# Kernel optimization log

Measured on AMD Instinct MI355X. Metric: run time of the kernel, lower is better.

The kernel has to match this reference:

```python
import jax, jax.numpy as jnp
import numpy as np

N = 100000        # vertices
E = 20000         # hyperedges
NNZ = 1000000     # incidence pairs
IN_CH = 128
HEADS = 8
OUT_CH = 16
D = HEADS * OUT_CH  # 128
NUM_TYPES = 16
K_CURV = 1.0      # Lorentz k = 1/c with c = 1


def lorentz_linear(x, W, b, scale_log):
    # HyboNet LorentzLinear: linear map, then project onto hyperboloid.
    y = x @ W.T + b                                   # [N, D]
    time = jax.nn.sigmoid(y[..., :1]) * jnp.exp(scale_log) + 1.1  # [N, 1]
    x_narrow = y[..., 1:]                             # [N, D-1]
    sq = jnp.sum(x_narrow * x_narrow, axis=-1, keepdims=True)
    scale = (time * time - K_CURV) / (sq + 1e-8)
    return jnp.concatenate([time, x_narrow * jnp.sqrt(scale)], axis=-1)


def setup_inputs() -> dict:
    key = jax.random.key(0)
    ks = jax.random.split(key, 8)
    X = jax.random.normal(ks[0], (N, IN_CH), dtype=jnp.float32)
    emb_ty = jax.random.normal(ks[1], (NUM_TYPES, D), dtype=jnp.float32)
    vertex = jax.random.randint(ks[2], (NNZ,), 0, N, dtype=jnp.int32)
    edges = jax.random.randint(ks[3], (NNZ,), 0, E, dtype=jnp.int32)
    type_ids = jax.random.randint(ks[4], (NNZ,), 0, NUM_TYPES, dtype=jnp.int32)
    # LorentzLinear params (nn.Linear with bias, scale init log(10))
    W = jax.random.normal(ks[5], (D, IN_CH), dtype=jnp.float32) / np.sqrt(IN_CH)
    b = jnp.zeros((D,), dtype=jnp.float32)
    scale_log = jnp.asarray(np.log(10.0), dtype=jnp.float32)
    eps = jnp.asarray([0.5], dtype=jnp.float32)
    return {"X": X, "emb_ty": emb_ty, "W": W, "b": b, "scale_log": scale_log,
            "eps": eps, "vertex": vertex, "edges": edges, "type_ids": type_ids,
            "num_edges": E}


def reference(X, emb_ty, W, b, scale_log, eps, vertex, edges, type_ids, num_edges):
    n = X.shape[0]
    Xh = lorentz_linear(X, W, b, scale_log)           # [N, D]
    Xve = Xh[vertex] - emb_ty[type_ids]               # [NNZ, D] gather + subtract
    Xe = jax.ops.segment_sum(Xve, edges, num_segments=num_edges)  # [E, D]
    Xev = Xe[edges]                                   # [NNZ, D]
    Xv = jax.ops.segment_sum(Xev, vertex, num_segments=n)         # [N, D]
    return eps * Xv + Xh
```

## Files before the change

### kernel.cpp

```cpp
#include <hip/hip_runtime.h>
#include <hip/hip_bf16.h>


#define E_SEGS 20000

__global__ __launch_bounds__(256) void lorentz_gemm_kernel(
    const float* __restrict__ X, const float* __restrict__ W,
    const float* __restrict__ bias, const float* __restrict__ scale_log,
    float* __restrict__ Xh, int N)
{
    __shared__ float Wt[128][132];
    __shared__ float Xs[128][64];
    const int t = threadIdx.x;

    #pragma unroll
    for (int i = 0; i < 16; ++i) {
        int f4 = t + i * 256;
        int d  = f4 >> 5;
        int k0 = (f4 & 31) << 2;
        float4 w = ((const float4*)W)[f4];
        Wt[k0+0][d] = w.x; Wt[k0+1][d] = w.y;
        Wt[k0+2][d] = w.z; Wt[k0+3][d] = w.w;
    }
    const int row0 = blockIdx.x * 64;
    #pragma unroll
    for (int i = 0; i < 8; ++i) {
        int f4 = t + i * 256;
        int r  = f4 >> 5;
        int k0 = (f4 & 31) << 2;
        int gr = row0 + r;
        float4 x = make_float4(0.f, 0.f, 0.f, 0.f);
        if (gr < N) x = ((const float4*)X)[(size_t)gr * 32 + (f4 & 31)];
        Xs[k0+0][r] = x.x; Xs[k0+1][r] = x.y;
        Xs[k0+2][r] = x.z; Xs[k0+3][r] = x.w;
    }
    __syncthreads();

    const int rg = t >> 4;
    const int cg = t & 15;
    const int cb = cg << 3;

    float acc[4][8];
    #pragma unroll
    for (int r = 0; r < 4; ++r)
        #pragma unroll
        for (int j = 0; j < 8; ++j) acc[r][j] = 0.f;

    #pragma unroll 4
    for (int k = 0; k < 128; ++k) {
        float4 xr = *(const float4*)&Xs[k][rg << 2];
        float4 w0 = *(const float4*)&Wt[k][cb];
        float4 w1 = *(const float4*)&Wt[k][cb + 4];
        #pragma unroll
        for (int r = 0; r < 4; ++r) {
            float xv = (&xr.x)[r];
            acc[r][0] += xv * w0.x; acc[r][1] += xv * w0.y;
            acc[r][2] += xv * w0.z; acc[r][3] += xv * w0.w;
            acc[r][4] += xv * w1.x; acc[r][5] += xv * w1.y;
            acc[r][6] += xv * w1.z; acc[r][7] += xv * w1.w;
        }
    }

    float4 b0 = ((const float4*)bias)[cg * 2];
    float4 b1 = ((const float4*)bias)[cg * 2 + 1];
    #pragma unroll
    for (int r = 0; r < 4; ++r) {
        acc[r][0] += b0.x; acc[r][1] += b0.y; acc[r][2] += b0.z; acc[r][3] += b0.w;
        acc[r][4] += b1.x; acc[r][5] += b1.y; acc[r][6] += b1.z; acc[r][7] += b1.w;
    }

    const float es = expf(scale_log[0]);

    #pragma unroll
    for (int r = 0; r < 4; ++r) {
        float sq = 0.f;
        #pragma unroll
        for (int j = 0; j < 8; ++j) sq += acc[r][j] * acc[r][j];
        if (cg == 0) sq -= acc[r][0] * acc[r][0];
        #pragma unroll
        for (int m = 1; m < 16; m <<= 1) sq += __shfl_xor(sq, m, 16);
        float y0   = __shfl(acc[r][0], 0, 16);
        float time = es / (1.f + expf(-y0)) + 1.1f;
        float ss   = sqrtf((time * time - 1.f) / (sq + 1e-8f));
        float4 o0, o1;
        o0.x = (cg == 0) ? time : acc[r][0] * ss;
        o0.y = acc[r][1] * ss; o0.z = acc[r][2] * ss; o0.w = acc[r][3] * ss;
        o1.x = acc[r][4] * ss; o1.y = acc[r][5] * ss;
        o1.z = acc[r][6] * ss; o1.w = acc[r][7] * ss;
        int grow = row0 + (rg << 2) + r;
        if (grow < N) {
            float4* ph = (float4*)(Xh + (size_t)grow * 128 + cb);
            ph[0] = o0; ph[1] = o1;
        }
    }
}

__global__ __launch_bounds__(256) void count_both_kernel(
    const int* __restrict__ edges, const int* __restrict__ vertex,
    int* __restrict__ hist_e, int* __restrict__ hist_v, int n)
{
    int i = blockIdx.x * 256 + threadIdx.x;
    if (i < n) {
        atomicAdd(&hist_e[edges[i]], 1);
        atomicAdd(&hist_v[vertex[i]], 1);
    }
}

__global__ __launch_bounds__(1024) void scan_kernel(
    const int* __restrict__ counts, int* __restrict__ offs, int n)
{
    __shared__ int buf[1024];
    __shared__ int s_carry;
    const int tid = threadIdx.x;
    if (tid == 0) s_carry = 0;
    __syncthreads();
    for (int base = 0; base < n; base += 4096) {
        int i0 = base + tid * 4;
        int c0 = (i0 + 0 < n) ? counts[i0 + 0] : 0;
        int c1 = (i0 + 1 < n) ? counts[i0 + 1] : 0;
        int c2 = (i0 + 2 < n) ? counts[i0 + 2] : 0;
        int c3 = (i0 + 3 < n) ? counts[i0 + 3] : 0;
        int s = c0 + c1 + c2 + c3;
        buf[tid] = s;
        __syncthreads();
        for (int off = 1; off < 1024; off <<= 1) {
            int t = (tid >= off) ? buf[tid - off] : 0;
            __syncthreads();
            buf[tid] += t;
            __syncthreads();
        }
        int incl  = buf[tid];
        int total = buf[1023];
        int carry = s_carry;
        int ex = carry + incl - s;
        if (i0 + 0 < n) offs[i0 + 0] = ex;
        if (i0 + 1 < n) offs[i0 + 1] = ex + c0;
        if (i0 + 2 < n) offs[i0 + 2] = ex + c0 + c1;
        if (i0 + 3 < n) offs[i0 + 3] = ex + c0 + c1 + c2;
        __syncthreads();
        if (tid == 0) s_carry = carry + total;
        __syncthreads();
    }
    if (tid == 0) offs[n] = s_carry;
}

__global__ __launch_bounds__(256) void fill_both_kernel(
    const int* __restrict__ edges, const int* __restrict__ vertex,
    const int* __restrict__ types,
    const int* __restrict__ offs_e, int* __restrict__ cur_e,
    int* __restrict__ vals_e,
    const int* __restrict__ offs_v, int* __restrict__ cur_v,
    int* __restrict__ segs_v, int n)
{
    int i = blockIdx.x * 256 + threadIdx.x;
    if (i < n) {
        int s = edges[i];
        int v = vertex[i];
        int pe = atomicAdd(&cur_e[s], 1);
        vals_e[offs_e[s] + pe] = v | (types[i] << 17);
        int pv = atomicAdd(&cur_v[v], 1);
        segs_v[offs_v[v] + pv] = s;
    }
}

__global__ __launch_bounds__(256) void edge_gather_kernel(
    const float* __restrict__ Xh, const float* __restrict__ emb,
    const int* __restrict__ offs, const int* __restrict__ vals,
    float* __restrict__ Xe, int nsegs)
{
    int seg = blockIdx.x * 4 + (threadIdx.x >> 6);
    if (seg >= nsegs) return;
    int lane = threadIdx.x & 63;
    int beg = offs[seg], end = offs[seg + 1];
    float2 acc = make_float2(0.f, 0.f);
    int e = beg;
    for (; e + 1 < end; e += 2) {
        int p0 = vals[e], p1 = vals[e + 1];
        int v0 = p0 & 0x1FFFF, t0 = p0 >> 17;
        int v1 = p1 & 0x1FFFF, t1 = p1 >> 17;
        float2 a  = ((const float2*)Xh)[(size_t)v0 * 64 + lane];
        float2 b  = ((const float2*)Xh)[(size_t)v1 * 64 + lane];
        float2 m0 = ((const float2*)emb)[t0 * 64 + lane];
        float2 m1 = ((const float2*)emb)[t1 * 64 + lane];
        acc.x += (a.x - m0.x) + (b.x - m1.x);
        acc.y += (a.y - m0.y) + (b.y - m1.y);
    }
    if (e < end) {
        int p0 = vals[e];
        int v0 = p0 & 0x1FFFF, t0 = p0 >> 17;
        float2 a  = ((const float2*)Xh)[(size_t)v0 * 64 + lane];
        float2 m0 = ((const float2*)emb)[t0 * 64 + lane];
        acc.x += a.x - m0.x;
        acc.y += a.y - m0.y;
    }
    ((float2*)Xe)[(size_t)seg * 64 + lane] = acc;
}

__global__ __launch_bounds__(256) void vertex_gather_kernel(
    const float* __restrict__ Xh, const float* __restrict__ Xe,
    const int* __restrict__ offs, const int* __restrict__ segs,
    const float* __restrict__ eps, float* __restrict__ out, int N)
{
    int v = blockIdx.x * 4 + (threadIdx.x >> 6);
    if (v >= N) return;
    int lane = threadIdx.x & 63;
    int beg = offs[v], end = offs[v + 1];
    float2 acc = make_float2(0.f, 0.f);
    int e = beg;
    for (; e + 1 < end; e += 2) {
        int s0 = segs[e], s1 = segs[e + 1];
        float2 a = ((const float2*)Xe)[(size_t)s0 * 64 + lane];
        float2 b = ((const float2*)Xe)[(size_t)s1 * 64 + lane];
        acc.x += a.x + b.x;
        acc.y += a.y + b.y;
    }
    if (e < end) {
        int s0 = segs[e];
        float2 a = ((const float2*)Xe)[(size_t)s0 * 64 + lane];
        acc.x += a.x;
        acc.y += a.y;
    }
    float ep = eps[0];
    float2 xh = ((const float2*)Xh)[(size_t)v * 64 + lane];
    float2 o;
    o.x = xh.x + ep * acc.x;
    o.y = xh.y + ep * acc.y;
    ((float2*)out)[(size_t)v * 64 + lane] = o;
}

extern "C" void kernel_launch(void* const* d_in, const int* in_sizes, int n_in,
                              void* d_out, int out_size, void* d_ws, size_t ws_size,
                              hipStream_t stream) {
    const float* X         = (const float*)d_in[0];
    const float* emb_ty    = (const float*)d_in[1];
    const float* W         = (const float*)d_in[2];
    const float* bias      = (const float*)d_in[3];
    const float* scale_log = (const float*)d_in[4];
    const float* eps       = (const float*)d_in[5];
    const int*   vertex    = (const int*)d_in[6];
    const int*   edges     = (const int*)d_in[7];
    const int*   type_ids  = (const int*)d_in[8];

    const int N   = in_sizes[0] / 128;
    const int nnz = in_sizes[6];
    const int E   = E_SEGS;

    float* Xh = (float*)d_ws;
    float* Xe = Xh + (size_t)N * 128;
    int* ip      = (int*)(Xe + (size_t)E * 128);
    int* offs_e  = ip;              ip += E + 1;
    int* offs_v  = ip;              ip += N + 1;
    int* hist_e  = ip;              ip += E;
    int* hist_v  = ip;              ip += N;
    int* cur_e   = ip;              ip += E;
    int* cur_v   = ip;              ip += N;
    int* vals_e  = ip;              ip += nnz;
    int* segs_v  = ip;              ip += nnz;

    hipMemsetAsync(hist_e, 0, (size_t)(2 * E + 2 * N) * sizeof(int), stream);

    float* out = (float*)d_out;
    int blocks_nnz = (nnz + 255) / 256;

    count_both_kernel<<<blocks_nnz, 256, 0, stream>>>(
        edges, vertex, hist_e, hist_v, nnz);
    scan_kernel<<<1, 1024, 0, stream>>>(hist_e, offs_e, E);
    scan_kernel<<<1, 1024, 0, stream>>>(hist_v, offs_v, N);
    fill_both_kernel<<<blocks_nnz, 256, 0, stream>>>(
        edges, vertex, type_ids, offs_e, cur_e, vals_e, offs_v, cur_v,
        segs_v, nnz);

    lorentz_gemm_kernel<<<(N + 63) / 64, 256, 0, stream>>>(
        X, W, bias, scale_log, Xh, N);

    edge_gather_kernel<<<(E + 3) / 4, 256, 0, stream>>>(
        Xh, emb_ty, offs_e, vals_e, Xe, E);

    vertex_gather_kernel<<<(N + 3) / 4, 256, 0, stream>>>(
        Xh, Xe, offs_v, segs_v, eps, out, N);
}
```

Baseline: 717.5 us.

## Parallelize prefix scans, swizzle GEMM smem, and widen gather loads to float4

The single-block scans over the edge and vertex histograms are replaced by a three-phase multi-block scan: partial scans, a scan of block sums, then an add pass. The GEMM now stores W and X row-major in shared memory as float4, with an XOR swizzle on W and padding on X, and computes dot products over k in groups of four. The edge and vertex gather kernels switch from float2 to float4 loads, with each half-wave taking alternate incidences and a shuffle combining the two halves. The scan change removes a serialized one-block bottleneck at the cost of extra launches, and the gather change halves the number of load instructions per row.

```diff
diff --git a/kernel.cpp b/kernel.cpp
--- a/kernel.cpp
+++ b/kernel.cpp
@@ -9,58 +9,59 @@
     const float* __restrict__ bias, const float* __restrict__ scale_log,
     float* __restrict__ Xh, int N)
 {
-    __shared__ float Wt[128][132];
-    __shared__ float Xs[128][64];
+    __shared__ float4 Ws[128 * 32];
+    __shared__ float4 Xs[64 * 33];
     const int t = threadIdx.x;
 
     #pragma unroll
     for (int i = 0; i < 16; ++i) {
         int f4 = t + i * 256;
         int d  = f4 >> 5;
-        int k0 = (f4 & 31) << 2;
-        float4 w = ((const float4*)W)[f4];
-        Wt[k0+0][d] = w.x; Wt[k0+1][d] = w.y;
-        Wt[k0+2][d] = w.z; Wt[k0+3][d] = w.w;
+        int c  = f4 & 31;
+        Ws[d * 32 + (c ^ ((d >> 3) & 7))] = ((const float4*)W)[f4];
     }
     const int row0 = blockIdx.x * 64;
     #pragma unroll
     for (int i = 0; i < 8; ++i) {
         int f4 = t + i * 256;
         int r  = f4 >> 5;
-        int k0 = (f4 & 31) << 2;
+        int c  = f4 & 31;
         int gr = row0 + r;
         float4 x = make_float4(0.f, 0.f, 0.f, 0.f);
-        if (gr < N) x = ((const float4*)X)[(size_t)gr * 32 + (f4 & 31)];
-        Xs[k0+0][r] = x.x; Xs[k0+1][r] = x.y;
-        Xs[k0+2][r] = x.z; Xs[k0+3][r] = x.w;
+        if (gr < N) x = ((const float4*)X)[(size_t)gr * 32 + c];
+        Xs[r * 33 + c] = x;
     }
     __syncthreads();
 
-    const int rg = t >> 4;
-    const int cg = t & 15;
+    const int rg  = t >> 4;
+    const int cg  = t & 15;
+    const int r0  = rg << 2;
+    const int swz = cg & 7;
+
+    float acc[4][8];
+    #pragma unroll
+    for (int r = 0; r < 4; ++r)
+        #pragma unroll
+        for (int j = 0; j < 8; ++j) acc[r][j] = 0.f;
+
+    #pragma unroll 2
+    for (int k4 = 0; k4 < 32; ++k4) {
+        float4 xq[4];
+        #pragma unroll
+        for (int rr = 0; rr < 4; ++rr) xq[rr] = Xs[(r0 + rr) * 33 + k4];
+        float4 wq[8];
+        const int kk = k4 ^ swz;
+        #pragma unroll
+        for (int j = 0; j < 8; ++j) wq[j] = Ws[(cg * 8 + j) * 32 + kk];
+        #pragma unroll
+        for (int rr = 0; rr < 4; ++rr)
+            #pragma unroll
+            for (int j = 0; j < 8; ++j)
+                acc[rr][j] += xq[rr].x * wq[j].x + xq[rr].y * wq[j].y
+                            + xq[rr].z * wq[j].z + xq[rr].w * wq[j].w;
+    }
+
     const int cb = cg << 3;
-
-    float acc[4][8];
-    #pragma unroll
-    for (int r = 0; r < 4; ++r)
-        #pragma unroll
-        for (int j = 0; j < 8; ++j) acc[r][j] = 0.f;
-
-    #pragma unroll 4
-    for (int k = 0; k < 128; ++k) {
-        float4 xr = *(const float4*)&Xs[k][rg << 2];
-        float4 w0 = *(const float4*)&Wt[k][cb];
-        float4 w1 = *(const float4*)&Wt[k][cb + 4];
-        #pragma unroll
-        for (int r = 0; r < 4; ++r) {
-            float xv = (&xr.x)[r];
-            acc[r][0] += xv * w0.x; acc[r][1] += xv * w0.y;
-            acc[r][2] += xv * w0.z; acc[r][3] += xv * w0.w;
-            acc[r][4] += xv * w1.x; acc[r][5] += xv * w1.y;
-            acc[r][6] += xv * w1.z; acc[r][7] += xv * w1.w;
-        }
-    }
-
     float4 b0 = ((const float4*)bias)[cg * 2];
     float4 b1 = ((const float4*)bias)[cg * 2 + 1];
     #pragma unroll
@@ -87,7 +88,7 @@
         o0.y = acc[r][1] * ss; o0.z = acc[r][2] * ss; o0.w = acc[r][3] * ss;
         o1.x = acc[r][4] * ss; o1.y = acc[r][5] * ss;
         o1.z = acc[r][6] * ss; o1.w = acc[r][7] * ss;
-        int grow = row0 + (rg << 2) + r;
+        int grow = row0 + r0 + r;
         if (grow < N) {
             float4* ph = (float4*)(Xh + (size_t)grow * 128 + cb);
             ph[0] = o0; ph[1] = o1;
@@ -106,42 +107,66 @@
     }
 }
 
-__global__ __launch_bounds__(1024) void scan_kernel(
-    const int* __restrict__ counts, int* __restrict__ offs, int n)
-{
-    __shared__ int buf[1024];
-    __shared__ int s_carry;
+__global__ __launch_bounds__(256) void scan_partial_kernel(
+    const int* __restrict__ counts, int* __restrict__ offs,
+    int* __restrict__ bsums, int n)
+{
+    __shared__ int buf[256];
+    const int b = blockIdx.x, tid = threadIdx.x;
+    const int i0 = b * 1024 + tid * 4;
+    int c0 = (i0 + 0 < n) ? counts[i0 + 0] : 0;
+    int c1 = (i0 + 1 < n) ? counts[i0 + 1] : 0;
+    int c2 = (i0 + 2 < n) ? counts[i0 + 2] : 0;
+    int c3 = (i0 + 3 < n) ? counts[i0 + 3] : 0;
+    int s = c0 + c1 + c2 + c3;
+    buf[tid] = s;
+    __syncthreads();
+    #pragma unroll
+    for (int off = 1; off < 256; off <<= 1) {
+        int v = (tid >= off) ? buf[tid - off] : 0;
+        __syncthreads();
+        buf[tid] += v;
+        __syncthreads();
+    }
+    int ex = buf[tid] - s;
+    if (i0 + 0 < n) offs[i0 + 0] = ex;
+    if (i0 + 1 < n) offs[i0 + 1] = ex + c0;
+    if (i0 + 2 < n) offs[i0 + 2] = ex + c0 + c1;
+    if (i0 + 3 < n) offs[i0 + 3] = ex + c0 + c1 + c2;
+    if (tid == 255) bsums[b] = buf[255];
+}
+
+__global__ __launch_bounds__(256) void scan_bsums_kernel(
+    int* __restrict__ bsums, int nb)
+{
+    __shared__ int buf[256];
     const int tid = threadIdx.x;
-    if (tid == 0) s_carry = 0;
+    int v = (tid < nb) ? bsums[tid] : 0;
+    buf[tid] = v;
     __syncthreads();
-    for (int base = 0; base < n; base += 4096) {
-        int i0 = base + tid * 4;
-        int c0 = (i0 + 0 < n) ? counts[i0 + 0] : 0;
-        int c1 = (i0 + 1 < n) ? counts[i0 + 1] : 0;
-        int c2 = (i0 + 2 < n) ? counts[i0 + 2] : 0;
-        int c3 = (i0 + 3 < n) ? counts[i0 + 3] : 0;
-        int s = c0 + c1 + c2 + c3;
-        buf[tid] = s;
+    #pragma unroll
+    for (int off = 1; off < 256; off <<= 1) {
+        int u = (tid >= off) ? buf[tid - off] : 0;
         __syncthreads();
-        for (int off = 1; off < 1024; off <<= 1) {
-            int t = (tid >= off) ? buf[tid - off] : 0;
-            __syncthreads();
-            buf[tid] += t;
-            __syncthreads();
-        }
-        int incl  = buf[tid];
-        int total = buf[1023];
-        int carry = s_carry;
-        int ex = carry + incl - s;
-        if (i0 + 0 < n) offs[i0 + 0] = ex;
-        if (i0 + 1 < n) offs[i0 + 1] = ex + c0;
-        if (i0 + 2 < n) offs[i0 + 2] = ex + c0 + c1;
-        if (i0 + 3 < n) offs[i0 + 3] = ex + c0 + c1 + c2;
+        buf[tid] += u;
         __syncthreads();
-        if (tid == 0) s_carry = carry + total;
-        __syncthreads();
-    }
-    if (tid == 0) offs[n] = s_carry;
+    }
+    if (tid < nb) bsums[tid] = buf[tid] - v;
+}
+
+__global__ __launch_bounds__(256) void scan_add_kernel(
+    int* __restrict__ offs, const int* __restrict__ bsums, int n, int total)
+{
+    const int b = blockIdx.x, tid = threadIdx.x;
+    const int add = bsums[b];
+    const int i0 = b * 1024 + tid * 4;
+    if (add != 0) {
+        if (i0 + 0 < n) offs[i0 + 0] += add;
+        if (i0 + 1 < n) offs[i0 + 1] += add;
+        if (i0 + 2 < n) offs[i0 + 2] += add;
+        if (i0 + 3 < n) offs[i0 + 3] += add;
+    }
+    if (b == 0 && tid == 0) offs[n] = total;
 }
 
 __global__ __launch_bounds__(256) void fill_both_kernel(
@@ -170,30 +195,23 @@
 {
     int seg = blockIdx.x * 4 + (threadIdx.x >> 6);
     if (seg >= nsegs) return;
-    int lane = threadIdx.x & 63;
-    int beg = offs[seg], end = offs[seg + 1];
-    float2 acc = make_float2(0.f, 0.f);
-    int e = beg;
-    for (; e + 1 < end; e += 2) {
-        int p0 = vals[e], p1 = vals[e + 1];
-        int v0 = p0 & 0x1FFFF, t0 = p0 >> 17;
-        int v1 = p1 & 0x1FFFF, t1 = p1 >> 17;
-        float2 a  = ((const float2*)Xh)[(size_t)v0 * 64 + lane];
-        float2 b  = ((const float2*)Xh)[(size_t)v1 * 64 + lane];
-        float2 m0 = ((const float2*)emb)[t0 * 64 + lane];
-        float2 m1 = ((const float2*)emb)[t1 * 64 + lane];
-        acc.x += (a.x - m0.x) + (b.x - m1.x);
-        acc.y += (a.y - m0.y) + (b.y - m1.y);
-    }
-    if (e < end) {
-        int p0 = vals[e];
-        int v0 = p0 & 0x1FFFF, t0 = p0 >> 17;
-        float2 a  = ((const float2*)Xh)[(size_t)v0 * 64 + lane];
-        float2 m0 = ((const float2*)emb)[t0 * 64 + lane];
-        acc.x += a.x - m0.x;
-        acc.y += a.y - m0.y;
-    }
-    ((float2*)Xe)[(size_t)seg * 64 + lane] = acc;
+    const int lane = threadIdx.x & 63;
+    const int h = lane >> 5, l5 = lane & 31;
+    const int beg = offs[seg], end = offs[seg + 1];
+    float4 acc = make_float4(0.f, 0.f, 0.f, 0.f);
+    for (int e = beg + h; e < end; e += 2) {
+        int p  = vals[e];
+        int v  = p & 0x1FFFF, ty = p >> 17;
+        float4 a = ((const float4*)Xh)[(size_t)v * 32 + l5];
+        float4 m = ((const float4*)emb)[ty * 32 + l5];
+        acc.x += a.x - m.x; acc.y += a.y - m.y;
+        acc.z += a.z - m.z; acc.w += a.w - m.w;
+    }
+    acc.x += __shfl_xor(acc.x, 32);
+    acc.y += __shfl_xor(acc.y, 32);
+    acc.z += __shfl_xor(acc.z, 32);
+    acc.w += __shfl_xor(acc.w, 32);
+    if (h == 0) ((float4*)Xe)[(size_t)seg * 32 + l5] = acc;
 }
 
 __global__ __launch_bounds__(256) void vertex_gather_kernel(
@@ -203,29 +221,27 @@
 {
     int v = blockIdx.x * 4 + (threadIdx.x >> 6);
     if (v >= N) return;
-    int lane = threadIdx.x & 63;
-    int beg = offs[v], end = offs[v + 1];
-    float2 acc = make_float2(0.f, 0.f);
-    int e = beg;
-    for (; e + 1 < end; e += 2) {
-        int s0 = segs[e], s1 = segs[e + 1];
-        float2 a = ((const float2*)Xe)[(size_t)s0 * 64 + lane];
-        float2 b = ((const float2*)Xe)[(size_t)s1 * 64 + lane];
-        acc.x += a.x + b.x;
-        acc.y += a.y + b.y;
-    }
-    if (e < end) {
-        int s0 = segs[e];
-        float2 a = ((const float2*)Xe)[(size_t)s0 * 64 + lane];
-        acc.x += a.x;
-        acc.y += a.y;
-    }
-    float ep = eps[0];
-    float2 xh = ((const float2*)Xh)[(size_t)v * 64 + lane];
-    float2 o;
-    o.x = xh.x + ep * acc.x;
-    o.y = xh.y + ep * acc.y;
-    ((float2*)out)[(size_t)v * 64 + lane] = o;
+    const int lane = threadIdx.x & 63;
+    const int h = lane >> 5, l5 = lane & 31;
+    const int beg = offs[v], end = offs[v + 1];
+    float4 acc = make_float4(0.f, 0.f, 0.f, 0.f);
+    for (int e = beg + h; e < end; e += 2) {
+        int s = segs[e];
+        float4 a = ((const float4*)Xe)[(size_t)s * 32 + l5];
+        acc.x += a.x; acc.y += a.y; acc.z += a.z; acc.w += a.w;
+    }
+    acc.x += __shfl_xor(acc.x, 32);
+    acc.y += __shfl_xor(acc.y, 32);
+    acc.z += __shfl_xor(acc.z, 32);
+    acc.w += __shfl_xor(acc.w, 32);
+    if (h == 0) {
+        float ep = eps[0];
+        float4 xh = ((const float4*)Xh)[(size_t)v * 32 + l5];
+        float4 o;
+        o.x = xh.x + ep * acc.x; o.y = xh.y + ep * acc.y;
+        o.z = xh.z + ep * acc.z; o.w = xh.w + ep * acc.w;
+        ((float4*)out)[(size_t)v * 32 + l5] = o;
+    }
 }
 
 extern "C" void kernel_launch(void* const* d_in, const int* in_sizes, int n_in,
@@ -254,18 +270,28 @@
     int* hist_v  = ip;              ip += N;
     int* cur_e   = ip;              ip += E;
     int* cur_v   = ip;              ip += N;
+    int* bsum_e  = ip;              ip += 256;
+    int* bsum_v  = ip;              ip += 256;
     int* vals_e  = ip;              ip += nnz;
     int* segs_v  = ip;              ip += nnz;
 
     hipMemsetAsync(hist_e, 0, (size_t)(2 * E + 2 * N) * sizeof(int), stream);
 
     float* out = (float*)d_out;
-    int blocks_nnz = (nnz + 255) / 256;
+    const int blocks_nnz = (nnz + 255) / 256;
+    const int nb_e = (E + 1023) / 1024;
+    const int nb_v = (N + 1023) / 1024;
 
     count_both_kernel<<<blocks_nnz, 256, 0, stream>>>(
         edges, vertex, hist_e, hist_v, nnz);
-    scan_kernel<<<1, 1024, 0, stream>>>(hist_e, offs_e, E);
-    scan_kernel<<<1, 1024, 0, stream>>>(hist_v, offs_v, N);
+
+    scan_partial_kernel<<<nb_e, 256, 0, stream>>>(hist_e, offs_e, bsum_e, E);
+    scan_partial_kernel<<<nb_v, 256, 0, stream>>>(hist_v, offs_v, bsum_v, N);
+    scan_bsums_kernel<<<1, 256, 0, stream>>>(bsum_e, nb_e);
+    scan_bsums_kernel<<<1, 256, 0, stream>>>(bsum_v, nb_v);
+    scan_add_kernel<<<nb_e, 256, 0, stream>>>(offs_e, bsum_e, E, nnz);
+    scan_add_kernel<<<nb_v, 256, 0, stream>>>(offs_v, bsum_v, N, nnz);
+
     fill_both_kernel<<<blocks_nnz, 256, 0, stream>>>(
         edges, vertex, type_ids, offs_e, cur_e, vals_e, offs_v, cur_v,
         segs_v, nnz);
```

Result: faster. 574.6 us (-19.9%).
